# Performance work log

Hardware: AMD Instinct MI355X
Metric: run time of the kernel (lower is better)

## Reference

```python
import jax, jax.numpy as jnp
import numpy as np

N_EMBD = 1024
HEAD_SIZE = 64
B, T = 8, 2048


def setup_inputs() -> dict:
    key = jax.random.key(0)
    k1, k2, k3, k4 = jax.random.split(key, 4)
    scale = 1.0 / np.sqrt(N_EMBD)
    return {
        "x": jax.random.normal(k1, (B, T, N_EMBD), dtype=jnp.float32),
        "Wq": jax.random.normal(k2, (N_EMBD, HEAD_SIZE), dtype=jnp.float32) * scale,
        "Wk": jax.random.normal(k3, (N_EMBD, HEAD_SIZE), dtype=jnp.float32) * scale,
        "Wv": jax.random.normal(k4, (N_EMBD, HEAD_SIZE), dtype=jnp.float32) * scale,
    }


def reference(x, Wq, Wk, Wv):
    # x: [B, T, C]; projections (no bias)
    q = jnp.einsum("btc,ch->bth", x, Wq)
    k = jnp.einsum("btc,ch->bth", x, Wk)
    v = jnp.einsum("btc,ch->bth", x, Wv)
    head_size = k.shape[-1]
    # scaled scores [B, T, T]
    wei = jnp.einsum("bth,bsh->bts", q, k) * (head_size ** -0.5)
    # causal mask (lower-triangular keeps)
    Tlen = x.shape[1]
    causal = jnp.tril(jnp.ones((Tlen, Tlen), dtype=bool))
    wei = jnp.where(causal[None, :, :], wei, -jnp.inf)
    wei = jax.nn.softmax(wei, axis=-1)
    # dropout p=0 (eval) -> identity
    out = jnp.einsum("bts,bsh->bth", wei, v)
    return out
```

## Files before the change

kernel.cpp:

```cpp
#include <hip/hip_runtime.h>
#include <hip/hip_bf16.h>
#include <math.h>

#define Bn 8
#define Tn 2048
#define Cn 1024
#define Hn 64

typedef __attribute__((ext_vector_type(8))) short short8;
typedef __attribute__((ext_vector_type(4))) float floatx4;

#define ATTN_SCALE 0.18033688011112042f

__device__ inline unsigned short f2bf(float f) {
    union { float f; unsigned int u; } x; x.f = f;
    unsigned int r = x.u + 0x7fffu + ((x.u >> 16) & 1u);
    return (unsigned short)(r >> 16);
}

__device__ inline uint2 pack4bf(float4 v) {
    __hip_bfloat162 lo = __float22bfloat162_rn(make_float2(v.x, v.y));
    __hip_bfloat162 hi = __float22bfloat162_rn(make_float2(v.z, v.w));
    uint2 r;
    r.x = *reinterpret_cast<unsigned int*>(&lo);
    r.y = *reinterpret_cast<unsigned int*>(&hi);
    return r;
}

__device__ inline float rsum16(float v) {
    v += __shfl_xor(v, 1);
    v += __shfl_xor(v, 2);
    v += __shfl_xor(v, 4);
    v += __shfl_xor(v, 8);
    return v;
}

__global__ __launch_bounds__(256) void prep_w(
    const float* __restrict__ Wq, const float* __restrict__ Wk,
    const float* __restrict__ Wv, unsigned short* __restrict__ Wfrag)
{
    const int gid = blockIdx.x * 256 + threadIdx.x;
    const int c    = gid >> 11;
    const int rem  = gid & 2047;
    const int ks   = rem >> 6;
    const int lane = rem & 63;
    const int ln = lane & 15, qd = lane >> 4;
    const int mat = c >> 2, nc = c & 3;
    const float* W = (mat == 0) ? Wq : (mat == 1) ? Wk : Wv;
    const float sc = (mat == 0) ? ATTN_SCALE : 1.0f;
    const int col = nc * 16 + ln;
    unsigned short o[8];
    #pragma unroll
    for (int j = 0; j < 8; ++j)
        o[j] = f2bf(W[(size_t)(ks * 32 + qd * 8 + j) * Hn + col] * sc);
    *reinterpret_cast<short8*>(Wfrag + (size_t)gid * 8) = *reinterpret_cast<short8*>(o);
}

__global__ __launch_bounds__(256, 4) void proj_mfma(
    const float* __restrict__ x, const unsigned short* __restrict__ Wfrag,
    unsigned short* __restrict__ qbf, unsigned short* __restrict__ kfrag,
    unsigned short* __restrict__ vfrag)
{
    __shared__ unsigned short xs[32 * 512];

    const int ln   = threadIdx.x & 15;
    const int quad = (threadIdx.x >> 4) & 3;
    const int w    = threadIdx.x >> 6;
    const int lane = threadIdx.x & 63;
    const int row0 = blockIdx.x * 16;

    const int srow = threadIdx.x >> 4;
    const int sf   = threadIdx.x & 15;
    const float4* xrow4 = reinterpret_cast<const float4*>(x + (size_t)(row0 + srow) * Cn);

    float4 ld[16];
    #pragma unroll
    for (int it = 0; it < 16; ++it)
        ld[it] = xrow4[sf + 16 * it];
    #pragma unroll
    for (int it = 0; it < 16; ++it) {
        const int f4g = sf + 16 * it;
        const int s = f4g >> 3;
        const int q = (f4g >> 1) & 3;
        const int j = (f4g & 1) * 4;
        *reinterpret_cast<uint2*>(&xs[s * 512 + (q * 16 + srow) * 8 + j]) = pack4bf(ld[it]);
    }
    __syncthreads();

    floatx4 acc[3];
    #pragma unroll
    for (int i = 0; i < 3; ++i) acc[i] = (floatx4){0.f, 0.f, 0.f, 0.f};

    #pragma unroll 4
    for (int s = 0; s < 32; ++s) {
        const short8 a = *reinterpret_cast<const short8*>(&xs[s * 512 + lane * 8]);
        #pragma unroll
        for (int i = 0; i < 3; ++i) {
            const int cc = w * 3 + i;
            const short8 b = *reinterpret_cast<const short8*>(
                Wfrag + ((size_t)(cc * 32 + s) * 64 + lane) * 8);
            acc[i] = __builtin_amdgcn_mfma_f32_16x16x32_bf16(a, b, acc[i], 0, 0, 0);
        }
    }

    const int t0   = row0 + quad * 4;
    const int b    = t0 >> 11;
    const int tloc = t0 & 2047;
    #pragma unroll
    for (int i = 0; i < 3; ++i) {
        const int idx = w * 3 + i;
        const int mat = idx >> 2, ch = idx & 3;
        if (mat == 0) {
            #pragma unroll
            for (int r = 0; r < 4; ++r)
                qbf[(size_t)(t0 + r) * Hn + ch * 16 + ln] = f2bf(acc[i][r]);
        } else if (mat == 1) {
            const int kc = tloc >> 4;
            const int ks = ch >> 1;
            const int lq = (ch & 1) * 2 + (ln >> 3);
            #pragma unroll
            for (int r = 0; r < 4; ++r) {
                const int lanep = (quad * 4 + r) + 16 * lq;
                kfrag[(((size_t)(b * 128 + kc) * 2 + ks) * 64 + lanep) * 8 + (ln & 7)]
                    = f2bf(acc[i][r]);
            }
        } else {
            const int kb32 = tloc >> 5;
            const int off  = t0 & 31;
            const int qd   = off >> 3;
            const int j0   = off & 7;
            const int lanep = ln + 16 * qd;
            ushort4 pk;
            pk.x = f2bf(acc[i][0]); pk.y = f2bf(acc[i][1]);
            pk.z = f2bf(acc[i][2]); pk.w = f2bf(acc[i][3]);
            *reinterpret_cast<ushort4*>(
                vfrag + (((size_t)(b * 64 + kb32) * 4 + ch) * 64 + lanep) * 8 + j0) = pk;
        }
    }
}

__global__ __launch_bounds__(256, 4) void attn_mfma(
    const unsigned short* __restrict__ qbf, const unsigned short* __restrict__ kfrag,
    const unsigned short* __restrict__ vt, float* __restrict__ out)
{
    __shared__ unsigned short p_lds[4][16 * 40];
    __shared__ float o_lds[4][16][68];
    __shared__ float l_lds[4][16];

    const int j  = blockIdx.x;
    const int b  = j & 7;
    const int ti = 127 - (j >> 3);
    const int q0 = ti * 16;

    const int ln   = threadIdx.x & 15;
    const int quad = (threadIdx.x >> 4) & 3;
    const int w    = threadIdx.x >> 6;
    const int lane = threadIdx.x & 63;

    const unsigned short* qb = qbf + (size_t)b * Tn * Hn;
    const unsigned short* Kb = kfrag + (size_t)b * 131072;
    const unsigned short* Vb = vt + (size_t)b * 131072;

    const short8 aq0 = *reinterpret_cast<const short8*>(qb + (size_t)(q0 + ln) * Hn + quad * 8);
    const short8 aq1 = *reinterpret_cast<const short8*>(qb + (size_t)(q0 + ln) * Hn + 32 + quad * 8);

    floatx4 O[4];
    #pragma unroll
    for (int c = 0; c < 4; ++c) O[c] = (floatx4){0.f, 0.f, 0.f, 0.f};
    float lp[4] = {0.f, 0.f, 0.f, 0.f};

    const int ntiles = (q0 + 47) >> 5;
    const int per    = (ntiles + 3) >> 2;
    const int beg    = w * per;
    const int end    = min(beg + per, ntiles);
    unsigned short* pP = p_lds[w];

    short8 kf[4];
    if (beg < end) {
        #pragma unroll
        for (int u = 0; u < 4; ++u)
            kf[u] = *reinterpret_cast<const short8*>(Kb + ((size_t)(beg * 4 + u)) * 512 + lane * 8);
    }

    for (int t = beg; t < end; ++t) {
        const int tn = (t + 1 < end) ? (t + 1) : t;
        short8 kn[4], vf[4];
        #pragma unroll
        for (int u = 0; u < 4; ++u) {
            kn[u] = *reinterpret_cast<const short8*>(Kb + ((size_t)(tn * 4 + u)) * 512 + lane * 8);
            vf[u] = *reinterpret_cast<const short8*>(Vb + ((size_t)(t * 4 + u)) * 512 + lane * 8);
        }

        const floatx4 z = (floatx4){0.f, 0.f, 0.f, 0.f};
        floatx4 S[2];
        #pragma unroll
        for (int s = 0; s < 2; ++s) {
            S[s] = __builtin_amdgcn_mfma_f32_16x16x32_bf16(aq0, kf[s * 2], z, 0, 0, 0);
            S[s] = __builtin_amdgcn_mfma_f32_16x16x32_bf16(aq1, kf[s * 2 + 1], S[s], 0, 0, 0);
        }

        const bool diag = (t == ntiles - 1);
        #pragma unroll
        for (int s = 0; s < 2; ++s) {
            #pragma unroll
            for (int r = 0; r < 4; ++r) {
                float sv = S[s][r];
                if (diag && (t * 32 + s * 16 + ln > q0 + quad * 4 + r)) sv = -1e30f;
                const unsigned int pu = __float_as_uint(exp2f(sv));
                lp[r] += __uint_as_float(pu & 0xffff0000u);
                pP[(quad * 4 + r) * 40 + s * 16 + ln] = (unsigned short)(pu >> 16);
            }
        }
        __asm__ volatile("s_waitcnt lgkmcnt(0)" ::: "memory");
        const short8 pa = *reinterpret_cast<const short8*>(pP + ln * 40 + quad * 8);
        #pragma unroll
        for (int c = 0; c < 4; ++c)
            O[c] = __builtin_amdgcn_mfma_f32_16x16x32_bf16(pa, vf[c], O[c], 0, 0, 0);
        #pragma unroll
        for (int u = 0; u < 4; ++u) kf[u] = kn[u];
    }

    #pragma unroll
    for (int c = 0; c < 4; ++c)
        #pragma unroll
        for (int r = 0; r < 4; ++r)
            o_lds[w][quad * 4 + r][c * 16 + ln] = O[c][r];
    #pragma unroll
    for (int r = 0; r < 4; ++r) {
        const float ls = rsum16(lp[r]);
        if (ln == 0) l_lds[w][quad * 4 + r] = ls;
    }
    __syncthreads();

    const int qq = threadIdx.x >> 4;
    const int dg = threadIdx.x & 15;
    const float ltot = l_lds[0][qq] + l_lds[1][qq] + l_lds[2][qq] + l_lds[3][qq];
    const float inv = 1.0f / ltot;
    const float4 a0 = *reinterpret_cast<float4*>(&o_lds[0][qq][dg * 4]);
    const float4 a1 = *reinterpret_cast<float4*>(&o_lds[1][qq][dg * 4]);
    const float4 a2 = *reinterpret_cast<float4*>(&o_lds[2][qq][dg * 4]);
    const float4 a3 = *reinterpret_cast<float4*>(&o_lds[3][qq][dg * 4]);
    float4 r;
    r.x = (a0.x + a1.x + a2.x + a3.x) * inv;
    r.y = (a0.y + a1.y + a2.y + a3.y) * inv;
    r.z = (a0.z + a1.z + a2.z + a3.z) * inv;
    r.w = (a0.w + a1.w + a2.w + a3.w) * inv;
    *reinterpret_cast<float4*>(out + ((size_t)b * Tn + q0 + qq) * Hn + dg * 4) = r;
}

extern "C" void kernel_launch(void* const* d_in, const int* in_sizes, int n_in,
                              void* d_out, int out_size, void* d_ws, size_t ws_size,
                              hipStream_t stream) {
    (void)in_sizes; (void)n_in; (void)out_size; (void)ws_size;
    const float* x  = (const float*)d_in[0];
    const float* Wq = (const float*)d_in[1];
    const float* Wk = (const float*)d_in[2];
    const float* Wv = (const float*)d_in[3];
    float* out = (float*)d_out;

    unsigned short* Wfrag = (unsigned short*)d_ws;
    unsigned short* qbf   = Wfrag + (size_t)196608;
    unsigned short* kfr   = qbf + (size_t)Bn * Tn * Hn;
    unsigned short* vfr   = kfr + (size_t)Bn * 131072;

    prep_w<<<96, 256, 0, stream>>>(Wq, Wk, Wv, Wfrag);
    proj_mfma<<<(Bn * Tn) / 16, 256, 0, stream>>>(x, Wfrag, qbf, kfr, vfr);
    attn_mfma<<<Bn * (Tn / 16), 256, 0, stream>>>(qbf, kfr, vfr, out);
}
```

Measured before the change: 125.0 us.

## Compute transposed scores to keep P in registers, use fp16 PV MFMA

The score tile is now computed transposed (K as the A operand), so each lane's four score outputs line up with the A-operand layout of a 16x16x16 fp16 MFMA. P therefore stays in registers instead of round-tripping through LDS with a waitcnt each iteration. V is stored as fp16 in a new 16-row fragment layout, the key tile shrinks from 32 to 16 so tile count equals ti+1, and the row-sum reduction changes accordingly. The cost is twice as many loop iterations, each with fewer MFMAs, and fp16 precision for P and V.

```diff
diff --git a/kernel.cpp b/kernel.cpp
--- a/kernel.cpp
+++ b/kernel.cpp
@@ -9,6 +9,7 @@
 
 typedef __attribute__((ext_vector_type(8))) short short8;
 typedef __attribute__((ext_vector_type(4))) float floatx4;
+typedef __attribute__((ext_vector_type(4))) _Float16 half4;
 
 #define ATTN_SCALE 0.18033688011112042f
 
@@ -25,14 +26,6 @@
     r.x = *reinterpret_cast<unsigned int*>(&lo);
     r.y = *reinterpret_cast<unsigned int*>(&hi);
     return r;
-}
-
-__device__ inline float rsum16(float v) {
-    v += __shfl_xor(v, 1);
-    v += __shfl_xor(v, 2);
-    v += __shfl_xor(v, 4);
-    v += __shfl_xor(v, 8);
-    return v;
 }
 
 __global__ __launch_bounds__(256) void prep_w(
@@ -125,25 +118,20 @@
                     = f2bf(acc[i][r]);
             }
         } else {
-            const int kb32 = tloc >> 5;
-            const int off  = t0 & 31;
-            const int qd   = off >> 3;
-            const int j0   = off & 7;
-            const int lanep = ln + 16 * qd;
-            ushort4 pk;
-            pk.x = f2bf(acc[i][0]); pk.y = f2bf(acc[i][1]);
-            pk.z = f2bf(acc[i][2]); pk.w = f2bf(acc[i][3]);
+            const int t16 = tloc >> 4;
+            union { _Float16 h[4]; ushort4 u; } cv;
+            cv.h[0] = (_Float16)acc[i][0]; cv.h[1] = (_Float16)acc[i][1];
+            cv.h[2] = (_Float16)acc[i][2]; cv.h[3] = (_Float16)acc[i][3];
             *reinterpret_cast<ushort4*>(
-                vfrag + (((size_t)(b * 64 + kb32) * 4 + ch) * 64 + lanep) * 8 + j0) = pk;
+                vfrag + (((size_t)(b * 128 + t16) * 4 + ch) * 64 + ln + 16 * quad) * 4) = cv.u;
         }
     }
 }
 
 __global__ __launch_bounds__(256, 4) void attn_mfma(
     const unsigned short* __restrict__ qbf, const unsigned short* __restrict__ kfrag,
-    const unsigned short* __restrict__ vt, float* __restrict__ out)
+    const unsigned short* __restrict__ vfrag, float* __restrict__ out)
 {
-    __shared__ unsigned short p_lds[4][16 * 40];
     __shared__ float o_lds[4][16][68];
     __shared__ float l_lds[4][16];
 
@@ -159,7 +147,7 @@
 
     const unsigned short* qb = qbf + (size_t)b * Tn * Hn;
     const unsigned short* Kb = kfrag + (size_t)b * 131072;
-    const unsigned short* Vb = vt + (size_t)b * 131072;
+    const unsigned short* Vb = vfrag + (size_t)b * 131072;
 
     const short8 aq0 = *reinterpret_cast<const short8*>(qb + (size_t)(q0 + ln) * Hn + quad * 8);
     const short8 aq1 = *reinterpret_cast<const short8*>(qb + (size_t)(q0 + ln) * Hn + 32 + quad * 8);
@@ -167,57 +155,53 @@
     floatx4 O[4];
     #pragma unroll
     for (int c = 0; c < 4; ++c) O[c] = (floatx4){0.f, 0.f, 0.f, 0.f};
-    float lp[4] = {0.f, 0.f, 0.f, 0.f};
-
-    const int ntiles = (q0 + 47) >> 5;
+    float lp = 0.f;
+
+    const int ntiles = ti + 1;
     const int per    = (ntiles + 3) >> 2;
     const int beg    = w * per;
     const int end    = min(beg + per, ntiles);
-    unsigned short* pP = p_lds[w];
-
-    short8 kf[4];
+
+    union U4 { ushort4 u; half4 h; };
+    short8 kf0, kf1; U4 vf[4];
     if (beg < end) {
-        #pragma unroll
-        for (int u = 0; u < 4; ++u)
-            kf[u] = *reinterpret_cast<const short8*>(Kb + ((size_t)(beg * 4 + u)) * 512 + lane * 8);
+        kf0 = *reinterpret_cast<const short8*>(Kb + (size_t)(beg * 2) * 512 + lane * 8);
+        kf1 = *reinterpret_cast<const short8*>(Kb + (size_t)(beg * 2 + 1) * 512 + lane * 8);
+        #pragma unroll
+        for (int c = 0; c < 4; ++c)
+            vf[c].u = *reinterpret_cast<const ushort4*>(Vb + (size_t)(beg * 4 + c) * 256 + lane * 4);
     }
 
     for (int t = beg; t < end; ++t) {
         const int tn = (t + 1 < end) ? (t + 1) : t;
-        short8 kn[4], vf[4];
-        #pragma unroll
-        for (int u = 0; u < 4; ++u) {
-            kn[u] = *reinterpret_cast<const short8*>(Kb + ((size_t)(tn * 4 + u)) * 512 + lane * 8);
-            vf[u] = *reinterpret_cast<const short8*>(Vb + ((size_t)(t * 4 + u)) * 512 + lane * 8);
+        short8 kn0, kn1; U4 vn[4];
+        kn0 = *reinterpret_cast<const short8*>(Kb + (size_t)(tn * 2) * 512 + lane * 8);
+        kn1 = *reinterpret_cast<const short8*>(Kb + (size_t)(tn * 2 + 1) * 512 + lane * 8);
+        #pragma unroll
+        for (int c = 0; c < 4; ++c)
+            vn[c].u = *reinterpret_cast<const ushort4*>(Vb + (size_t)(tn * 4 + c) * 256 + lane * 4);
+
+        const floatx4 z = (floatx4){0.f, 0.f, 0.f, 0.f};
+        floatx4 St = __builtin_amdgcn_mfma_f32_16x16x32_bf16(kf0, aq0, z, 0, 0, 0);
+        St = __builtin_amdgcn_mfma_f32_16x16x32_bf16(kf1, aq1, St, 0, 0, 0);
+
+        const bool diag = (t == ntiles - 1);
+        half4 pa;
+        #pragma unroll
+        for (int r = 0; r < 4; ++r) {
+            float sv = St[r];
+            if (diag && (quad * 4 + r > ln)) sv = -1e30f;
+            const float p = exp2f(sv);
+            lp += p;
+            pa[r] = (_Float16)p;
         }
-
-        const floatx4 z = (floatx4){0.f, 0.f, 0.f, 0.f};
-        floatx4 S[2];
-        #pragma unroll
-        for (int s = 0; s < 2; ++s) {
-            S[s] = __builtin_amdgcn_mfma_f32_16x16x32_bf16(aq0, kf[s * 2], z, 0, 0, 0);
-            S[s] = __builtin_amdgcn_mfma_f32_16x16x32_bf16(aq1, kf[s * 2 + 1], S[s], 0, 0, 0);
-        }
-
-        const bool diag = (t == ntiles - 1);
-        #pragma unroll
-        for (int s = 0; s < 2; ++s) {
-            #pragma unroll
-            for (int r = 0; r < 4; ++r) {
-                float sv = S[s][r];
-                if (diag && (t * 32 + s * 16 + ln > q0 + quad * 4 + r)) sv = -1e30f;
-                const unsigned int pu = __float_as_uint(exp2f(sv));
-                lp[r] += __uint_as_float(pu & 0xffff0000u);
-                pP[(quad * 4 + r) * 40 + s * 16 + ln] = (unsigned short)(pu >> 16);
-            }
-        }
-        __asm__ volatile("s_waitcnt lgkmcnt(0)" ::: "memory");
-        const short8 pa = *reinterpret_cast<const short8*>(pP + ln * 40 + quad * 8);
         #pragma unroll
         for (int c = 0; c < 4; ++c)
-            O[c] = __builtin_amdgcn_mfma_f32_16x16x32_bf16(pa, vf[c], O[c], 0, 0, 0);
-        #pragma unroll
-        for (int u = 0; u < 4; ++u) kf[u] = kn[u];
+            O[c] = __builtin_amdgcn_mfma_f32_16x16x16f16(pa, vf[c].h, O[c], 0, 0, 0);
+
+        kf0 = kn0; kf1 = kn1;
+        #pragma unroll
+        for (int c = 0; c < 4; ++c) vf[c] = vn[c];
     }
 
     #pragma unroll
@@ -225,10 +209,11 @@
         #pragma unroll
         for (int r = 0; r < 4; ++r)
             o_lds[w][quad * 4 + r][c * 16 + ln] = O[c][r];
-    #pragma unroll
-    for (int r = 0; r < 4; ++r) {
-        const float ls = rsum16(lp[r]);
-        if (ln == 0) l_lds[w][quad * 4 + r] = ls;
+    {
+        float lt = lp;
+        lt += __shfl_xor(lt, 16);
+        lt += __shfl_xor(lt, 32);
+        if (quad == 0) l_lds[w][ln] = lt;
     }
     __syncthreads();
 
```

Measured after the change: 129.3 us. 1.03x slower.
